# Kernel optimization log

Measured on AMD Instinct MI355X. Metric: run time of the kernel, lower is better.

Reference implementation:

```python
import jax, jax.numpy as jnp
import numpy as np

N, E, C5, C6, H = 50000, 100000, 8000, 12000, 128
RE, R5, R6 = 2 * E, 5 * C5, 6 * C6
BN_EPS = 1e-5


def _bn_relu(x, g, b):
    # BatchNorm1d (training-mode batch stats, biased var) + ReLU
    m = x.mean(0)
    xc = x - m
    v = (xc * xc).mean(0)
    return jax.nn.relu(xc * jax.lax.rsqrt(v + BN_EPS) * g + b)


def _mlp2(x, w1, g1, b1, w2, g2, b2):
    h = _bn_relu(x @ w1, g1, b1)
    return _bn_relu(h @ w2, g2, b2)


def _gather11(x, src_nodes, src_inst, n_inst, tgt_nodes):
    # ptens 1b->1b gather (channel multiplier 2):
    #  part A: identity map on shared atoms, summed over overlapping sources
    #  part B: broadcast of source-instance sum to shared atoms
    pa = jax.ops.segment_sum(x, src_nodes, num_segments=N)[tgt_nodes]
    s = jax.ops.segment_sum(x, src_inst, num_segments=n_inst)
    pb = jax.ops.segment_sum(s[src_inst], src_nodes, num_segments=N)[tgt_nodes]
    return jnp.concatenate([pa, pb], -1)


def _forward(node_rep, edge_rep, cycle_rep, edge_nodes, c5_nodes, c6_nodes, P):
    (nm_w1, nm_g1, nm_b1, nm_w2, nm_g2, nm_b2,
     em_w1, em_g1, em_b1, em_w2, em_g2, em_b2,
     ce_w1, ce_g1, ce_b1, ce_w2, ce_g2, ce_b2,
     cm_w1, cm_g1, cm_b1, cm_w2, cm_g2, cm_b2,
     fm_w, fm_g, fm_b) = P
    edge_inst = jnp.arange(RE, dtype=jnp.int32) // 2
    c5_inst = jnp.arange(R5, dtype=jnp.int32) // 5
    c6_inst = jnp.arange(R6, dtype=jnp.int32) // 6
    cyc_nodes = jnp.concatenate([c5_nodes, c6_nodes])
    cyc_inst = jnp.concatenate([c5_inst, c6_inst + C5])

    # ---- Edge_node ----
    n2e = node_rep[edge_nodes]                                        # 0b->1b(edge), h
    n2e = _gather11(n2e, edge_nodes, edge_inst, E, edge_nodes)        # 2h
    e2e = _gather11(edge_rep, edge_nodes, edge_inst, E, edge_nodes)   # 2h
    e2e = _gather11(e2e, edge_nodes, edge_inst, E, edge_nodes)        # 4h
    e2n = jax.ops.segment_sum(jnp.concatenate([e2e, n2e], -1), edge_nodes, num_segments=N)  # 1b->0b, 6h
    edge_out1 = _mlp2(jnp.concatenate([edge_rep, e2e, n2e], -1),
                      em_w1, em_g1, em_b1, em_w2, em_g2, em_b2)       # [RE, h]
    node_out = _mlp2(jnp.concatenate([node_rep, e2n], -1),
                     nm_w1, nm_g1, nm_b1, nm_w2, nm_g2, nm_b2)        # [N, h]

    # ---- Edge_Cycle ----
    e2c5 = _gather11(edge_rep, edge_nodes, edge_inst, E, c5_nodes)    # 2h
    e2c5 = _gather11(e2c5, c5_nodes, c5_inst, C5, c5_nodes)           # 4h
    e2c6 = _gather11(edge_rep, edge_nodes, edge_inst, E, c6_nodes)    # 2h
    e2c6 = _gather11(e2c6, c6_nodes, c6_inst, C6, c6_nodes)           # 4h
    cycle_in = jnp.concatenate([e2c5, e2c6], 0)                       # row-cat: [R5+R6, 4h]
    cycle_new = jnp.concatenate([cycle_in, cycle_rep], -1)            # 5h
    c2e = _gather11(cycle_new, cyc_nodes, cyc_inst, C5 + C6, edge_nodes)  # 10h
    edge_out2 = _mlp2(jnp.concatenate([edge_rep, c2e], -1),
                      ce_w1, ce_g1, ce_b1, ce_w2, ce_g2, ce_b2)       # [RE, h]
    cycle_out = _mlp2(cycle_new, cm_w1, cm_g1, cm_b1, cm_w2, cm_g2, cm_b2)  # [R5+R6, h]

    edge_out = _bn_relu(jnp.concatenate([edge_out1, edge_out2], -1) @ fm_w, fm_g, fm_b)
    return node_out, edge_out, cycle_out


def setup_inputs() -> dict:
    key = jax.random.key(0)
    ks = jax.random.split(key, 16)
    d = {}
    d["node_rep"] = jax.random.normal(ks[0], (N, H), jnp.float32)
    d["edge_rep"] = jax.random.normal(ks[1], (RE, H), jnp.float32)
    d["cycle_rep"] = jax.random.normal(ks[2], (R5 + R6, H), jnp.float32)
    d["edge_nodes"] = jax.random.randint(ks[3], (RE,), 0, N, jnp.int32)
    d["c5_nodes"] = jax.random.randint(ks[4], (R5,), 0, N, jnp.int32)
    d["c6_nodes"] = jax.random.randint(ks[5], (R6,), 0, N, jnp.int32)
    i = [6]
    def w(shape):
        out = jax.random.normal(ks[i[0]], shape, jnp.float32) / np.float32(np.sqrt(shape[0]))
        i[0] += 1
        return out
    for p, fin in (("nm", 7 * H), ("em", 7 * H), ("ce", 11 * H), ("cm", 5 * H)):
        d[p + "_w1"] = w((fin, 2 * H)); d[p + "_g1"] = jnp.ones((2 * H,), jnp.float32); d[p + "_b1"] = jnp.zeros((2 * H,), jnp.float32)
        d[p + "_w2"] = w((2 * H, H)); d[p + "_g2"] = jnp.ones((H,), jnp.float32); d[p + "_b2"] = jnp.zeros((H,), jnp.float32)
    d["fm_w"] = w((2 * H, H)); d["fm_g"] = jnp.ones((H,), jnp.float32); d["fm_b"] = jnp.zeros((H,), jnp.float32)
    return d


def reference(node_rep, edge_rep, cycle_rep, edge_nodes, c5_nodes, c6_nodes,
              nm_w1, nm_g1, nm_b1, nm_w2, nm_g2, nm_b2,
              em_w1, em_g1, em_b1, em_w2, em_g2, em_b2,
              ce_w1, ce_g1, ce_b1, ce_w2, ce_g2, ce_b2,
              cm_w1, cm_g1, cm_b1, cm_w2, cm_g2, cm_b2,
              fm_w, fm_g, fm_b):
    P = (nm_w1, nm_g1, nm_b1, nm_w2, nm_g2, nm_b2,
         em_w1, em_g1, em_b1, em_w2, em_g2, em_b2,
         ce_w1, ce_g1, ce_b1, ce_w2, ce_g2, ce_b2,
         cm_w1, cm_g1, cm_b1, cm_w2, cm_g2, cm_b2,
         fm_w, fm_g, fm_b)
    return _forward(node_rep, edge_rep, cycle_rep, edge_nodes, c5_nodes, c6_nodes, P)
```

## Files before the change

kernel.cpp:

```cpp
#include <hip/hip_runtime.h>
#include <cstdint>
#include <cstddef>
#include <initializer_list>

typedef short bf16x8 __attribute__((ext_vector_type(8)));
typedef float f32x4 __attribute__((ext_vector_type(4)));

__device__ inline float bf2f(unsigned short h) { return __uint_as_float(((unsigned)h) << 16); }
__device__ inline unsigned short f2bf(float f) {
  unsigned u = __float_as_uint(f);
  u += 0x7fff + ((u >> 16) & 1);
  return (unsigned short)(u >> 16);
}

struct Seg { const void* base; const int* idx; const float* scale; int ld; int wk; int bf16;
             const float* bnsc; const float* bnsh; };
struct GemmArgs { Seg segs[7]; const float* addB; const int* addIdx; float* stats; int addBf16; };

__global__ void k_count(float* dst, const int* __restrict__ idx, int R) {
  int r = blockIdx.x * 256 + threadIdx.x;
  if (r < R) atomicAdd(&dst[idx[r]], 1.0f);
}

__global__ void k_scales(const float* __restrict__ deg, const float* __restrict__ d5,
                         const float* __restrict__ d6, float* deg2, float* dd, int n) {
  int i = blockIdx.x * 256 + threadIdx.x;
  if (i < n) {
    float d = deg[i]; deg2[i] = d * d;
    float a = d5[i], b = d6[i]; dd[i] = a * a + b * b;
  }
}

__global__ void k_wtrans(const float* __restrict__ W, unsigned short* __restrict__ Wt,
                         int K, int CN) {
  int t = blockIdx.x * 256 + threadIdx.x;
  if (t >= K * CN) return;
  int k = t / CN, n = t - k * CN;
  Wt[(size_t)n * K + k] = f2bf(W[t]);
}

__global__ void k_cvt(unsigned short* __restrict__ dst, const float* __restrict__ src, int n8) {
  int i = blockIdx.x * 256 + threadIdx.x;
  if (i >= n8) return;
  const float4* s = (const float4*)(src + (size_t)i * 8);
  float4 a = s[0], b = s[1];
  union { unsigned short u[8]; uint4 v; } o;
  o.u[0] = f2bf(a.x); o.u[1] = f2bf(a.y); o.u[2] = f2bf(a.z); o.u[3] = f2bf(a.w);
  o.u[4] = f2bf(b.x); o.u[5] = f2bf(b.y); o.u[6] = f2bf(b.z); o.u[7] = f2bf(b.w);
  *(uint4*)(dst + (size_t)i * 8) = o.v;
}

__global__ void k_gsum(float* __restrict__ out, int outLd,
                       const float* __restrict__ T, int tLd,
                       const float* __restrict__ scale, const int* __restrict__ idx,
                       int k, int nInst) {
  int t = blockIdx.x * 256 + threadIdx.x;
  int c = t >> 7, ch = t & 127;
  if (c >= nInst) return;
  float acc = 0.f;
  int b0 = c * k;
  for (int j = 0; j < k; ++j) {
    int rid = idx ? idx[b0 + j] : b0 + j;
    float v = T[(size_t)rid * tLd + ch];
    if (scale) v *= scale[rid];
    acc += v;
  }
  out[(size_t)c * outLd + ch] = acc;
}

__global__ void k_gsc(float* __restrict__ dst, const float* __restrict__ T1,
                      const float* __restrict__ T2, const int* __restrict__ gidx,
                      const int* __restrict__ sidx, int k, int nInst, int cshift) {
  int t = blockIdx.x * 256 + threadIdx.x;
  int c = t >> cshift;
  int C = 1 << cshift;
  int ch = t & (C - 1);
  if (c >= nInst) return;
  const float* T = (ch < 128) ? T1 : T2;
  int ch7 = ch & 127;
  float acc = 0.f;
  int b0 = c * k;
  for (int j = 0; j < k; ++j) {
    int rid = gidx ? gidx[b0 + j] : b0 + j;
    acc += T[(size_t)rid * 128 + ch7];
  }
  for (int j = 0; j < k; ++j)
    atomicAdd(&dst[(size_t)sidx[b0 + j] * C + ch], acc);
}

__global__ void k_scatter(float* __restrict__ dst, const float* __restrict__ src,
                          const int* __restrict__ idx, int R, int C, int div) {
  int r = blockIdx.x;
  if (r >= R) return;
  int n = idx[r];
  const float* s = src + (size_t)(r / div) * C;
  float* d = dst + (size_t)n * C;
  for (int c = threadIdx.x; c < C; c += blockDim.x)
    atomicAdd(&d[c], s[c]);
}

__global__ void k_bnfin(float* __restrict__ coef, const float* __restrict__ stats,
                        const float* __restrict__ g, const float* __restrict__ b,
                        int M, int C) {
  int c = threadIdx.x;
  if (c >= C) return;
  float s = 0.f, q = 0.f;
  for (int sh = 0; sh < 16; ++sh) { s += stats[sh * 512 + c]; q += stats[sh * 512 + 256 + c]; }
  float inv = 1.f / (float)M;
  float m = s * inv;
  float v = q * inv - m * m;
  float sc = g[c] * rsqrtf(v + 1e-5f);
  coef[c] = sc;
  coef[C + c] = b[c] - m * sc;
}

template <int OUT_BF16>
__launch_bounds__(256)
__global__ void k_gemm(GemmArgs ga, const unsigned short* __restrict__ Wt, int Ktot,
                       int K, int CN, void* __restrict__ Cp, int M) {
  __shared__ char AsB[2 * 128 * 64];
  __shared__ char BsB[2 * 128 * 64];
  int tid = threadIdx.x;
  int row0 = blockIdx.x * 128, col0 = blockIdx.y * 128;
  int l = tid & 63, w = tid >> 6;
  int wm = w >> 1, wn = w & 1;
  int lr = l & 15, g = l >> 4;
  int chunkOff = (g ^ ((lr >> 1) & 3)) << 4;
  int sm = tid >> 2;
  int sc4 = tid & 3;
  f32x4 acc[4][4] = {};

  uint4 pa0[2], pa1[2], pb[2];
  float psc[2];
  float4 c0, c1, c2, c3;

  auto issue = [&](int k0n) {
    Seg sg = ga.segs[k0n >> 7];
    int kin = k0n & 127;
#pragma unroll
    for (int h = 0; h < 2; ++h) {
      int m = sm + 64 * h;
      int grow = row0 + m;
      uint4 z4 = make_uint4(0, 0, 0, 0);
      pa0[h] = z4; pa1[h] = z4; psc[h] = 1.f;
      if (grow < M) {
        int rid = sg.idx ? sg.idx[grow] : grow;
        if (sg.bf16) {
          pa0[h] = *(const uint4*)((const unsigned short*)sg.base + (size_t)rid * sg.ld + kin + sc4 * 8);
        } else {
          const float* fp = (const float*)sg.base + (size_t)rid * sg.ld + kin + sc4 * 8;
          pa0[h] = *(const uint4*)fp;
          pa1[h] = *(const uint4*)(fp + 4);
          if (sg.scale) psc[h] = sg.scale[rid];
        }
      }
      pb[h] = *(const uint4*)(Wt + (size_t)(col0 + m) * Ktot + sg.wk + kin + sc4 * 8);
    }
    if (sg.bnsc) {
      const float* sp = sg.bnsc + kin + sc4 * 8;
      const float* hp = sg.bnsh + kin + sc4 * 8;
      c0 = *(const float4*)sp; c1 = *(const float4*)(sp + 4);
      c2 = *(const float4*)hp; c3 = *(const float4*)(hp + 4);
    }
  };

  issue(0);
  int buf = 0;
  for (int k0 = 0; k0 < K; k0 += 32) {
    {
      Seg sg = ga.segs[k0 >> 7];
      char* sA = AsB + buf * 8192;
      char* sB = BsB + buf * 8192;
#pragma unroll
      for (int h = 0; h < 2; ++h) {
        int m = sm + 64 * h;
        uint4 pk;
        if (sg.bf16) {
          pk = pa0[h];
          if (sg.bnsc) {
            unsigned short* u = (unsigned short*)&pk;
            float cs0[8] = {c0.x, c0.y, c0.z, c0.w, c1.x, c1.y, c1.z, c1.w};
            float sh0[8] = {c2.x, c2.y, c2.z, c2.w, c3.x, c3.y, c3.z, c3.w};
#pragma unroll
            for (int e = 0; e < 8; ++e) {
              float f = fmaxf(0.f, bf2f(u[e]) * cs0[e] + sh0[e]);
              u[e] = f2bf(f);
            }
          }
        } else {
          float4 v0 = *(const float4*)&pa0[h];
          float4 v1 = *(const float4*)&pa1[h];
          float s = psc[h];
          v0.x *= s; v0.y *= s; v0.z *= s; v0.w *= s;
          v1.x *= s; v1.y *= s; v1.z *= s; v1.w *= s;
          if (sg.bnsc) {
            v0.x = fmaxf(0.f, v0.x * c0.x + c2.x);
            v0.y = fmaxf(0.f, v0.y * c0.y + c2.y);
            v0.z = fmaxf(0.f, v0.z * c0.z + c2.z);
            v0.w = fmaxf(0.f, v0.w * c0.w + c2.w);
            v1.x = fmaxf(0.f, v1.x * c1.x + c3.x);
            v1.y = fmaxf(0.f, v1.y * c1.y + c3.y);
            v1.z = fmaxf(0.f, v1.z * c1.z + c3.z);
            v1.w = fmaxf(0.f, v1.w * c1.w + c3.w);
          }
          pk.x = f2bf(v0.x) | ((unsigned)f2bf(v0.y) << 16);
          pk.y = f2bf(v0.z) | ((unsigned)f2bf(v0.w) << 16);
          pk.z = f2bf(v1.x) | ((unsigned)f2bf(v1.y) << 16);
          pk.w = f2bf(v1.z) | ((unsigned)f2bf(v1.w) << 16);
        }
        *(uint4*)(sA + m * 64 + ((sc4 ^ ((m >> 1) & 3)) << 4)) = pk;
        *(uint4*)(sB + m * 64 + ((sc4 ^ ((m >> 1) & 3)) << 4)) = pb[h];
      }
    }
    __syncthreads();
    if (k0 + 32 < K) issue(k0 + 32);
    const char* lA = AsB + buf * 8192;
    const char* lB = BsB + buf * 8192;
    bf16x8 a[4], b4[4];
#pragma unroll
    for (int i = 0; i < 4; ++i) {
      int m = wm * 64 + i * 16 + lr;
      a[i] = *(const bf16x8*)(lA + m * 64 + chunkOff);
    }
#pragma unroll
    for (int j = 0; j < 4; ++j) {
      int n = wn * 64 + j * 16 + lr;
      b4[j] = *(const bf16x8*)(lB + n * 64 + chunkOff);
    }
#pragma unroll
    for (int i = 0; i < 4; ++i)
#pragma unroll
      for (int j = 0; j < 4; ++j)
        acc[i][j] = __builtin_amdgcn_mfma_f32_16x16x32_bf16(a[i], b4[j], acc[i][j], 0, 0, 0);
    buf ^= 1;
  }

  float csum[4] = {0.f, 0.f, 0.f, 0.f}, cqum[4] = {0.f, 0.f, 0.f, 0.f};
#pragma unroll
  for (int i = 0; i < 4; ++i) {
#pragma unroll
    for (int r = 0; r < 4; ++r) {
      int grow = row0 + wm * 64 + i * 16 + g * 4 + r;
      if (grow >= M) continue;
      const float* zrF = nullptr;
      const unsigned short* zrH = nullptr;
      if (ga.addB) {
        int rid = ga.addIdx ? ga.addIdx[grow] : grow;
        if (ga.addBf16) zrH = (const unsigned short*)ga.addB + (size_t)rid * 256;
        else            zrF = ga.addB + (size_t)rid * 256;
      }
#pragma unroll
      for (int j = 0; j < 4; ++j) {
        int col = col0 + wn * 64 + j * 16 + lr;
        float o = acc[i][j][r];
        if (zrF) o += zrF[col];
        if (zrH) o += bf2f(zrH[col]);
        csum[j] += o; cqum[j] += o * o;
        if (OUT_BF16) ((unsigned short*)Cp)[(size_t)grow * CN + col] = f2bf(o);
        else          ((float*)Cp)[(size_t)grow * CN + col] = o;
      }
    }
  }
  if (ga.stats) {
    int shard = (blockIdx.x & 15) * 512;
#pragma unroll
    for (int j = 0; j < 4; ++j) {
      float s = csum[j], q = cqum[j];
      s += __shfl_xor(s, 16); q += __shfl_xor(q, 16);
      s += __shfl_xor(s, 32); q += __shfl_xor(q, 32);
      if (g == 0) {
        int col = col0 + wn * 64 + j * 16 + lr;
        atomicAdd(&ga.stats[shard + col], s);
        atomicAdd(&ga.stats[shard + 256 + col], q);
      }
    }
  }
}

template <int SB, int DB>
__global__ void k_bnapply(void* __restrict__ dst, const void* __restrict__ yv,
                          const float* __restrict__ coef, int M, int C) {
  int t = blockIdx.x * 256 + threadIdx.x;
  if (t >= M * C) return;
  int c = t & (C - 1);
  float x = SB ? bf2f(((const unsigned short*)yv)[t]) : ((const float*)yv)[t];
  x = x * coef[c] + coef[C + c];
  x = x > 0.f ? x : 0.f;
  if (DB) ((unsigned short*)dst)[t] = f2bf(x);
  else    ((float*)dst)[t] = x;
}

extern "C" void kernel_launch(void* const* d_in, const int* in_sizes, int n_in,
                              void* d_out, int out_size, void* d_ws, size_t ws_size,
                              hipStream_t stream) {
  constexpr int N = 50000, E = 100000, C5 = 8000, C6 = 12000;
  constexpr int RE = 2 * E, R5 = 5 * C5, R6 = 6 * C6, NC = R5 + R6, CC = C5 + C6;

  const float* node_rep  = (const float*)d_in[0];
  const float* edge_rep  = (const float*)d_in[1];
  const float* cycle_rep = (const float*)d_in[2];
  const int* en  = (const int*)d_in[3];
  const int* cn5 = (const int*)d_in[4];
  const int* cn6 = (const int*)d_in[5];
  const float* nm_w1 = (const float*)d_in[6],  *nm_g1 = (const float*)d_in[7],  *nm_b1 = (const float*)d_in[8];
  const float* nm_w2 = (const float*)d_in[9],  *nm_g2 = (const float*)d_in[10], *nm_b2 = (const float*)d_in[11];
  const float* em_w1 = (const float*)d_in[12], *em_g1 = (const float*)d_in[13], *em_b1 = (const float*)d_in[14];
  const float* em_w2 = (const float*)d_in[15], *em_g2 = (const float*)d_in[16], *em_b2 = (const float*)d_in[17];
  const float* ce_w1 = (const float*)d_in[18], *ce_g1 = (const float*)d_in[19], *ce_b1 = (const float*)d_in[20];
  const float* ce_w2 = (const float*)d_in[21], *ce_g2 = (const float*)d_in[22], *ce_b2 = (const float*)d_in[23];
  const float* cm_w1 = (const float*)d_in[24], *cm_g1 = (const float*)d_in[25], *cm_b1 = (const float*)d_in[26];
  const float* cm_w2 = (const float*)d_in[27], *cm_g2 = (const float*)d_in[28], *cm_b2 = (const float*)d_in[29];
  const float* fm_w  = (const float*)d_in[30], *fm_g  = (const float*)d_in[31], *fm_b  = (const float*)d_in[32];
  float* outD = (float*)d_out;
  float* outN = outD;
  float* outE = outD + (size_t)N * 128;
  float* outC = outD + (size_t)(N + RE) * 128;

  char* wsb = (char*)d_ws;
  size_t off = 0;
  auto A = [&](size_t bytes) { void* p = wsb + off; off += (bytes + 255) & ~(size_t)255; return p; };
  float* deg = (float*)A(N * 4);
  float* d5  = (float*)A(N * 4);
  float* d6  = (float*)A(N * 4);
  float* Ae  = (float*)A((size_t)N * 128 * 4);
  float* Be  = (float*)A((size_t)N * 128 * 4);
  float* Bn  = (float*)A((size_t)N * 128 * 4);
  float* pb2 = (float*)A((size_t)N * 256 * 4);
  float* pb5 = (float*)A((size_t)N * 256 * 4);
  float* pb6 = (float*)A((size_t)N * 256 * 4);
  float* Ac  = (float*)A((size_t)N * 128 * 4);
  size_t zeroBytes = off;
  float* deg2 = (float*)A(N * 4);
  float* dd   = (float*)A(N * 4);
  float* Z    = (float*)A((size_t)N * 256 * 4);
  float* stats = (float*)A(16 * 512 * 4);
  float* coefCe1 = (float*)A(512 * 4);
  float* coefCe2 = (float*)A(512 * 4);
  float* coefEm1 = (float*)A(512 * 4);
  float* coefEm2 = (float*)A(512 * 4);
  float* coefNm1 = (float*)A(512 * 4);
  float* coefNm2 = (float*)A(512 * 4);
  float* coefCm1 = (float*)A(512 * 4);
  float* coefCm2 = (float*)A(512 * 4);
  float* coefFm  = (float*)A(512 * 4);
  unsigned short* WtNm1 = (unsigned short*)A((size_t)896 * 256 * 2);
  unsigned short* WtEm1 = (unsigned short*)A((size_t)896 * 256 * 2);
  unsigned short* WtCe1 = (unsigned short*)A((size_t)1408 * 256 * 2);
  unsigned short* WtCm1 = (unsigned short*)A((size_t)640 * 256 * 2);
  unsigned short* WtNm2 = (unsigned short*)A((size_t)256 * 128 * 2);
  unsigned short* WtEm2 = (unsigned short*)A((size_t)256 * 128 * 2);
  unsigned short* WtCe2 = (unsigned short*)A((size_t)256 * 128 * 2);
  unsigned short* WtCm2 = (unsigned short*)A((size_t)256 * 128 * 2);
  unsigned short* WtFm  = (unsigned short*)A((size_t)256 * 128 * 2);
  char*  Yb   = (char*)A((size_t)RE * 256 * 2);
  unsigned short* O2 = (unsigned short*)A((size_t)RE * 128 * 2);
  if (off > ws_size) return;

  unsigned short* Zb = (unsigned short*)Ac;

  float* scb = (float*)Yb;
  float* Ysc = scb + (size_t)CC * 640;

  auto gsum = [&](float* o, int oLd, const float* T, int tLd,
                  const float* scl, const int* idx, int k, int nInst) {
    int tot = nInst * 128;
    k_gsum<<<(tot + 255) / 256, 256, 0, stream>>>(o, oLd, T, tLd, scl, idx, k, nInst);
  };
  auto gsc = [&](float* dst, const float* T1, const float* T2, const int* gidx,
                 const int* sidx, int k, int nInst) {
    int cshift = T2 ? 8 : 7;
    int tot = nInst << cshift;
    k_gsc<<<(tot + 255) / 256, 256, 0, stream>>>(dst, T1, T2, gidx, sidx, k, nInst, cshift);
  };
  auto scat = [&](float* dst, const float* src, const int* idx, int R, int C, int dv) {
    k_scatter<<<R, 128, 0, stream>>>(dst, src, idx, R, C, dv);
  };
  auto wtr = [&](const float* W, unsigned short* Wt, int K, int CN) {
    k_wtrans<<<(K * CN + 255) / 256, 256, 0, stream>>>(W, Wt, K, CN);
  };
  auto gemm = [&](std::initializer_list<Seg> segs, const unsigned short* Wt, int Ktot,
                  int CN, void* Co, int M, bool outBf, const float* addB, const int* addIdx,
                  int addBf, float* st) {
    GemmArgs ga{}; int i = 0;
    for (const Seg& s : segs) ga.segs[i++] = s;
    ga.addB = addB; ga.addIdx = addIdx; ga.stats = st; ga.addBf16 = addBf;
    int K = i * 128;
    dim3 g((M + 127) / 128, CN / 128);
    if (outBf) k_gemm<1><<<g, 256, 0, stream>>>(ga, Wt, Ktot, K, CN, Co, M);
    else       k_gemm<0><<<g, 256, 0, stream>>>(ga, Wt, Ktot, K, CN, Co, M);
  };
  auto zstat = [&]() { hipMemsetAsync(stats, 0, 16 * 512 * sizeof(float), stream); };
  auto fin = [&](float* coef, const float* g, const float* b, int M, int C) {
    k_bnfin<<<1, 256, 0, stream>>>(coef, stats, g, b, M, C);
  };
  auto apply = [&](void* dst, const void* y, const float* coef, int M, int C, int sb, int db) {
    int tot = M * C, gb = (tot + 255) / 256;
    if (sb && db)       k_bnapply<1, 1><<<gb, 256, 0, stream>>>(dst, y, coef, M, C);
    else if (sb && !db) k_bnapply<1, 0><<<gb, 256, 0, stream>>>(dst, y, coef, M, C);
    else if (!sb && db) k_bnapply<0, 1><<<gb, 256, 0, stream>>>(dst, y, coef, M, C);
    else                k_bnapply<0, 0><<<gb, 256, 0, stream>>>(dst, y, coef, M, C);
  };

  hipMemsetAsync(d_ws, 0, zeroBytes, stream);
  k_count<<<(RE + 255) / 256, 256, 0, stream>>>(deg, en, RE);
  k_count<<<(R5 + 255) / 256, 256, 0, stream>>>(d5, cn5, R5);
  k_count<<<(R6 + 255) / 256, 256, 0, stream>>>(d6, cn6, R6);
  k_scales<<<(N + 255) / 256, 256, 0, stream>>>(deg, d5, d6, deg2, dd, N);
  wtr(nm_w1, WtNm1, 896, 256);  wtr(em_w1, WtEm1, 896, 256);
  wtr(ce_w1, WtCe1, 1408, 256); wtr(cm_w1, WtCm1, 640, 256);
  wtr(nm_w2, WtNm2, 256, 128);  wtr(em_w2, WtEm2, 256, 128);
  wtr(ce_w2, WtCe2, 256, 128);  wtr(cm_w2, WtCm2, 256, 128);
  wtr(fm_w,  WtFm,  256, 128);

  scat(Ae, edge_rep, en, RE, 128, 1);
  gsc(Be, edge_rep, nullptr, nullptr, en, 2, E);
  gsc(Bn, node_rep, nullptr, en, en, 2, E);
  gsc(pb2, Ae, Be, en, en, 2, E);

  gsc(pb5, Ae, Be, cn5, cn5, 5, C5);
  gsc(pb6, Ae, Be, cn6, cn6, 6, C6);
  scat(Ac, cycle_rep, cn5, R5, 128, 1);
  scat(Ac, cycle_rep + (size_t)R5 * 128, cn6, R6, 128, 1);

  gsum(scb + 0,   640, Ae, 128, d5, cn5, 5, C5);
  gsum(scb + 128, 640, Be, 128, d5, cn5, 5, C5);
  gsum(scb + 256, 640, pb5, 256, nullptr, cn5, 5, C5);
  gsum(scb + 384, 640, pb5 + 128, 256, nullptr, cn5, 5, C5);
  gsum(scb + 512, 640, cycle_rep, 128, nullptr, nullptr, 5, C5);
  float* sc6 = scb + (size_t)C5 * 640;
  gsum(sc6 + 0,   640, Ae, 128, d6, cn6, 6, C6);
  gsum(sc6 + 128, 640, Be, 128, d6, cn6, 6, C6);
  gsum(sc6 + 256, 640, pb6, 256, nullptr, cn6, 6, C6);
  gsum(sc6 + 384, 640, pb6 + 128, 256, nullptr, cn6, 6, C6);
  gsum(sc6 + 512, 640, cycle_rep + (size_t)R5 * 128, 128, nullptr, nullptr, 6, C6);
  gemm({{scb, nullptr, nullptr, 640, 768, 0}, {scb + 128, nullptr, nullptr, 640, 896, 0},
        {scb + 256, nullptr, nullptr, 640, 1024, 0}, {scb + 384, nullptr, nullptr, 640, 1152, 0},
        {scb + 512, nullptr, nullptr, 640, 1280, 0}},
       WtCe1, 1408, 256, Ysc, CC, false, nullptr, nullptr, 0, nullptr);
  gemm({{Ae, nullptr, dd, 128, 128, 0}, {Be, nullptr, dd, 128, 256, 0},
        {pb5, nullptr, d5, 256, 384, 0}, {pb5 + 128, nullptr, d5, 256, 512, 0},
        {pb6, nullptr, d6, 256, 384, 0}, {pb6 + 128, nullptr, d6, 256, 512, 0},
        {Ac, nullptr, nullptr, 128, 640, 0}},
       WtCe1, 1408, 256, Z, N, false, nullptr, nullptr, 0, nullptr);
  scat(Z, Ysc, cn5, R5, 256, 5);
  scat(Z, Ysc + (size_t)C5 * 256, cn6, R6, 256, 6);
  k_cvt<<<(N * 256 / 8 + 255) / 256, 256, 0, stream>>>(Zb, Z, N * 256 / 8);
  zstat();
  gemm({{edge_rep, nullptr, nullptr, 128, 0, 0}}, WtCe1, 1408, 256, Yb, RE, true,
       (const float*)Zb, en, 1, stats);
  fin(coefCe1, ce_g1, ce_b1, RE, 256);
  zstat();
  gemm({{Yb, nullptr, nullptr, 256, 0, 1, coefCe1, coefCe1 + 256},
        {Yb + 256, nullptr, nullptr, 256, 128, 1, coefCe1 + 128, coefCe1 + 384}},
       WtCe2, 256, 128, O2, RE, true, nullptr, nullptr, 0, stats);
  fin(coefCe2, ce_g2, ce_b2, RE, 128);

  gemm({{Ae, nullptr, deg, 128, 128, 0}, {Be, nullptr, deg, 128, 256, 0},
        {pb2, nullptr, nullptr, 256, 384, 0}, {pb2 + 128, nullptr, nullptr, 256, 512, 0},
        {node_rep, nullptr, deg, 128, 640, 0}, {Bn, nullptr, nullptr, 128, 768, 0}},
       WtEm1, 896, 256, Zb, N, true, nullptr, nullptr, 0, nullptr);
  zstat();
  gemm({{edge_rep, nullptr, nullptr, 128, 0, 0}}, WtEm1, 896, 256, Yb, RE, true,
       (const float*)Zb, en, 1, stats);
  fin(coefEm1, em_g1, em_b1, RE, 256);
  zstat();
  gemm({{Yb, nullptr, nullptr, 256, 0, 1, coefEm1, coefEm1 + 256},
        {Yb + 256, nullptr, nullptr, 256, 128, 1, coefEm1 + 128, coefEm1 + 384}},
       WtEm2, 256, 128, outE, RE, false, nullptr, nullptr, 0, stats);
  fin(coefEm2, em_g2, em_b2, RE, 128);

  zstat();
  gemm({{node_rep, nullptr, nullptr, 128, 0, 0}, {Ae, nullptr, deg2, 128, 128, 0},
        {Be, nullptr, deg2, 128, 256, 0}, {pb2, nullptr, deg, 256, 384, 0},
        {pb2 + 128, nullptr, deg, 256, 512, 0}, {node_rep, nullptr, deg2, 128, 640, 0},
        {Bn, nullptr, deg, 128, 768, 0}},
       WtNm1, 896, 256, Yb, N, true, nullptr, nullptr, 0, stats);
  fin(coefNm1, nm_g1, nm_b1, N, 256);
  zstat();
  gemm({{Yb, nullptr, nullptr, 256, 0, 1, coefNm1, coefNm1 + 256},
        {Yb + 256, nullptr, nullptr, 256, 128, 1, coefNm1 + 128, coefNm1 + 384}},
       WtNm2, 256, 128, outN, N, false, nullptr, nullptr, 0, stats);
  fin(coefNm2, nm_g2, nm_b2, N, 128);
  apply(outN, outN, coefNm2, N, 128, 0, 0);

  gemm({{Ae, nullptr, d5, 128, 0, 0}, {Be, nullptr, d5, 128, 128, 0},
        {pb5, nullptr, nullptr, 256, 256, 0}, {pb5 + 128, nullptr, nullptr, 256, 384, 0}},
       WtCm1, 640, 256, Zb, N, true, nullptr, nullptr, 0, nullptr);
  zstat();
  gemm({{cycle_rep, nullptr, nullptr, 128, 512, 0}}, WtCm1, 640, 256, Yb, R5, true,
       (const float*)Zb, cn5, 1, stats);
  gemm({{Ae, nullptr, d6, 128, 0, 0}, {Be, nullptr, d6, 128, 128, 0},
        {pb6, nullptr, nullptr, 256, 256, 0}, {pb6 + 128, nullptr, nullptr, 256, 384, 0}},
       WtCm1, 640, 256, Zb, N, true, nullptr, nullptr, 0, nullptr);
  gemm({{cycle_rep + (size_t)R5 * 128, nullptr, nullptr, 128, 512, 0}}, WtCm1, 640, 256,
       Yb + (size_t)R5 * 256 * 2, R6, true, (const float*)Zb, cn6, 1, stats);
  fin(coefCm1, cm_g1, cm_b1, NC, 256);
  zstat();
  gemm({{Yb, nullptr, nullptr, 256, 0, 1, coefCm1, coefCm1 + 256},
        {Yb + 256, nullptr, nullptr, 256, 128, 1, coefCm1 + 128, coefCm1 + 384}},
       WtCm2, 256, 128, outC, NC, false, nullptr, nullptr, 0, stats);
  fin(coefCm2, cm_g2, cm_b2, NC, 128);
  apply(outC, outC, coefCm2, NC, 128, 0, 0);

  zstat();
  gemm({{outE, nullptr, nullptr, 128, 0, 0, coefEm2, coefEm2 + 128},
        {O2, nullptr, nullptr, 128, 128, 1, coefCe2, coefCe2 + 128}},
       WtFm, 256, 128, Yb, RE, true, nullptr, nullptr, 0, stats);
  fin(coefFm, fm_g, fm_b, RE, 128);
  apply(outE, Yb, coefFm, RE, 128, 1, 0);
}
```

Baseline: 2.871 ms.

## Build CSR adjacency and replace atomic scatters with gather kernels in bf16

After: 2.796 ms. 2.6% less time.

```diff
diff --git a/kernel.cpp b/kernel.cpp
--- a/kernel.cpp
+++ b/kernel.cpp
@@ -17,17 +17,48 @@
              const float* bnsc; const float* bnsh; };
 struct GemmArgs { Seg segs[7]; const float* addB; const int* addIdx; float* stats; int addBf16; };
 
-__global__ void k_count(float* dst, const int* __restrict__ idx, int R) {
+__global__ void k_hist(int* cnt, const int* __restrict__ idx, int R) {
   int r = blockIdx.x * 256 + threadIdx.x;
-  if (r < R) atomicAdd(&dst[idx[r]], 1.0f);
-}
-
-__global__ void k_scales(const float* __restrict__ deg, const float* __restrict__ d5,
-                         const float* __restrict__ d6, float* deg2, float* dd, int n) {
+  if (r < R) atomicAdd(&cnt[idx[r]], 1);
+}
+
+__global__ void k_scan(int* __restrict__ cnt, int* __restrict__ off, int n) {
+  __shared__ int part[1024];
+  int t = threadIdx.x;
+  int chunk = (n + 1023) >> 10;
+  int b0 = t * chunk, b1 = min(n, b0 + chunk);
+  int s = 0;
+  for (int i = b0; i < b1; ++i) s += cnt[i];
+  part[t] = s;
+  __syncthreads();
+  for (int d = 1; d < 1024; d <<= 1) {
+    int v = (t >= d) ? part[t - d] : 0;
+    __syncthreads();
+    part[t] += v;
+    __syncthreads();
+  }
+  int run = t ? part[t - 1] : 0;
+  for (int i = b0; i < b1; ++i) { off[i] = run; run += cnt[i]; cnt[i] = 0; }
+  if (t == 1023) off[n] = part[1023];
+}
+
+__global__ void k_fill(int* __restrict__ adj, int* __restrict__ cur,
+                       const int* __restrict__ off, const int* __restrict__ idx, int R) {
+  int r = blockIdx.x * 256 + threadIdx.x;
+  if (r >= R) return;
+  int n = idx[r];
+  int p = atomicAdd(&cur[n], 1);
+  adj[off[n] + p] = r;
+}
+
+__global__ void k_scales(const int* __restrict__ ce, const int* __restrict__ c5,
+                         const int* __restrict__ c6, float* deg, float* d5, float* d6,
+                         float* deg2, float* dd, int n) {
   int i = blockIdx.x * 256 + threadIdx.x;
   if (i < n) {
-    float d = deg[i]; deg2[i] = d * d;
-    float a = d5[i], b = d6[i]; dd[i] = a * a + b * b;
+    float d = (float)ce[i]; deg[i] = d; deg2[i] = d * d;
+    float a = (float)c5[i], b = (float)c6[i];
+    d5[i] = a; d6[i] = b; dd[i] = a * a + b * b;
   }
 }
 
@@ -50,8 +81,9 @@
   *(uint4*)(dst + (size_t)i * 8) = o.v;
 }
 
-__global__ void k_gsum(float* __restrict__ out, int outLd,
-                       const float* __restrict__ T, int tLd,
+template <int SBF>
+__global__ void k_gsum(unsigned short* __restrict__ out, int outLd,
+                       const void* __restrict__ T, int tLd,
                        const float* __restrict__ scale, const int* __restrict__ idx,
                        int k, int nInst) {
   int t = blockIdx.x * 256 + threadIdx.x;
@@ -61,42 +93,114 @@
   int b0 = c * k;
   for (int j = 0; j < k; ++j) {
     int rid = idx ? idx[b0 + j] : b0 + j;
-    float v = T[(size_t)rid * tLd + ch];
+    float v = SBF ? bf2f(((const unsigned short*)T)[(size_t)rid * tLd + ch])
+                  : ((const float*)T)[(size_t)rid * tLd + ch];
     if (scale) v *= scale[rid];
     acc += v;
   }
-  out[(size_t)c * outLd + ch] = acc;
-}
-
-__global__ void k_gsc(float* __restrict__ dst, const float* __restrict__ T1,
-                      const float* __restrict__ T2, const int* __restrict__ gidx,
-                      const int* __restrict__ sidx, int k, int nInst, int cshift) {
-  int t = blockIdx.x * 256 + threadIdx.x;
-  int c = t >> cshift;
-  int C = 1 << cshift;
-  int ch = t & (C - 1);
-  if (c >= nInst) return;
-  const float* T = (ch < 128) ? T1 : T2;
+  out[(size_t)c * outLd + ch] = f2bf(acc);
+}
+
+__global__ void k_csr_ae(unsigned short* __restrict__ out, const float* __restrict__ src,
+                         const int* __restrict__ off, const int* __restrict__ adj, int n) {
+  int t = blockIdx.x * 256 + threadIdx.x;
+  int node = t >> 7, ch = t & 127;
+  if (node >= n) return;
+  float a = 0.f;
+  int p0 = off[node], p1 = off[node + 1];
+  for (int p = p0; p < p1; ++p) a += src[(size_t)adj[p] * 128 + ch];
+  out[(size_t)node * 128 + ch] = f2bf(a);
+}
+
+__global__ void k_csr_be(unsigned short* __restrict__ out, const float* __restrict__ src,
+                         const int* __restrict__ off, const int* __restrict__ adj, int n) {
+  int t = blockIdx.x * 256 + threadIdx.x;
+  int node = t >> 7, ch = t & 127;
+  if (node >= n) return;
+  float a = 0.f;
+  int p0 = off[node], p1 = off[node + 1];
+  for (int p = p0; p < p1; ++p) {
+    int e2 = adj[p] & ~1;
+    a += src[(size_t)e2 * 128 + ch] + src[(size_t)(e2 + 1) * 128 + ch];
+  }
+  out[(size_t)node * 128 + ch] = f2bf(a);
+}
+
+__global__ void k_csr_bn(unsigned short* __restrict__ out, const float* __restrict__ src,
+                         const int* __restrict__ en, const int* __restrict__ off,
+                         const int* __restrict__ adj, int n) {
+  int t = blockIdx.x * 256 + threadIdx.x;
+  int node = t >> 7, ch = t & 127;
+  if (node >= n) return;
+  float a = 0.f;
+  int p0 = off[node], p1 = off[node + 1];
+  for (int p = p0; p < p1; ++p) {
+    int e2 = adj[p] & ~1;
+    a += src[(size_t)en[e2] * 128 + ch] + src[(size_t)en[e2 + 1] * 128 + ch];
+  }
+  out[(size_t)node * 128 + ch] = f2bf(a);
+}
+
+__global__ void k_csr_p2(unsigned short* __restrict__ out, const unsigned short* __restrict__ AeB,
+                         const unsigned short* __restrict__ BeB, const int* __restrict__ en,
+                         const int* __restrict__ off, const int* __restrict__ adj, int n) {
+  int t = blockIdx.x * 256 + threadIdx.x;
+  int node = t >> 8, ch = t & 255;
+  if (node >= n) return;
+  const unsigned short* Tab = (ch < 128) ? AeB : BeB;
   int ch7 = ch & 127;
-  float acc = 0.f;
-  int b0 = c * k;
-  for (int j = 0; j < k; ++j) {
-    int rid = gidx ? gidx[b0 + j] : b0 + j;
-    acc += T[(size_t)rid * 128 + ch7];
-  }
-  for (int j = 0; j < k; ++j)
-    atomicAdd(&dst[(size_t)sidx[b0 + j] * C + ch], acc);
-}
-
-__global__ void k_scatter(float* __restrict__ dst, const float* __restrict__ src,
-                          const int* __restrict__ idx, int R, int C, int div) {
-  int r = blockIdx.x;
-  if (r >= R) return;
-  int n = idx[r];
-  const float* s = src + (size_t)(r / div) * C;
-  float* d = dst + (size_t)n * C;
-  for (int c = threadIdx.x; c < C; c += blockDim.x)
-    atomicAdd(&d[c], s[c]);
+  float a = 0.f;
+  int p0 = off[node], p1 = off[node + 1];
+  for (int p = p0; p < p1; ++p) {
+    int e2 = adj[p] & ~1;
+    a += bf2f(Tab[(size_t)en[e2] * 128 + ch7]) + bf2f(Tab[(size_t)en[e2 + 1] * 128 + ch7]);
+  }
+  out[(size_t)node * 256 + ch] = f2bf(a);
+}
+
+template <int KK>
+__global__ void k_csr_p56(unsigned short* __restrict__ out, const unsigned short* __restrict__ AeB,
+                          const unsigned short* __restrict__ BeB, const int* __restrict__ cn,
+                          const int* __restrict__ off, const int* __restrict__ adj, int n) {
+  int t = blockIdx.x * 256 + threadIdx.x;
+  int node = t >> 8, ch = t & 255;
+  if (node >= n) return;
+  const unsigned short* Tab = (ch < 128) ? AeB : BeB;
+  int ch7 = ch & 127;
+  float a = 0.f;
+  int p0 = off[node], p1 = off[node + 1];
+  for (int p = p0; p < p1; ++p) {
+    int b = (adj[p] / KK) * KK;
+#pragma unroll
+    for (int j = 0; j < KK; ++j) a += bf2f(Tab[(size_t)cn[b + j] * 128 + ch7]);
+  }
+  out[(size_t)node * 256 + ch] = f2bf(a);
+}
+
+__global__ void k_csr_ac(unsigned short* __restrict__ out, const float* __restrict__ cyc,
+                         const int* __restrict__ off5, const int* __restrict__ adj5,
+                         const int* __restrict__ off6, const int* __restrict__ adj6,
+                         int r5off, int n) {
+  int t = blockIdx.x * 256 + threadIdx.x;
+  int node = t >> 7, ch = t & 127;
+  if (node >= n) return;
+  float a = 0.f;
+  for (int p = off5[node]; p < off5[node + 1]; ++p) a += cyc[(size_t)adj5[p] * 128 + ch];
+  for (int p = off6[node]; p < off6[node + 1]; ++p) a += cyc[(size_t)(r5off + adj6[p]) * 128 + ch];
+  out[(size_t)node * 128 + ch] = f2bf(a);
+}
+
+__global__ void k_zmerge(unsigned short* __restrict__ Zb, const float* __restrict__ Ysc5,
+                         const float* __restrict__ Ysc6,
+                         const int* __restrict__ off5, const int* __restrict__ adj5,
+                         const int* __restrict__ off6, const int* __restrict__ adj6, int n) {
+  int t = blockIdx.x * 256 + threadIdx.x;
+  int node = t >> 8, ch = t & 255;
+  if (node >= n) return;
+  float a = bf2f(Zb[(size_t)node * 256 + ch]);
+  for (int p = off5[node]; p < off5[node + 1]; ++p) a += Ysc5[(size_t)(adj5[p] / 5) * 256 + ch];
+  for (int p = off6[node]; p < off6[node + 1]; ++p) a += Ysc6[(size_t)(adj6[p] / 6) * 256 + ch];
+  Zb[(size_t)node * 256 + ch] = f2bf(a);
 }
 
 __global__ void k_bnfin(float* __restrict__ coef, const float* __restrict__ stats,
@@ -147,6 +251,7 @@
         int rid = sg.idx ? sg.idx[grow] : grow;
         if (sg.bf16) {
           pa0[h] = *(const uint4*)((const unsigned short*)sg.base + (size_t)rid * sg.ld + kin + sc4 * 8);
+          if (sg.scale) psc[h] = sg.scale[rid];
         } else {
           const float* fp = (const float*)sg.base + (size_t)rid * sg.ld + kin + sc4 * 8;
           pa0[h] = *(const uint4*)fp;
@@ -186,6 +291,11 @@
               float f = fmaxf(0.f, bf2f(u[e]) * cs0[e] + sh0[e]);
               u[e] = f2bf(f);
             }
+          } else if (sg.scale) {
+            unsigned short* u = (unsigned short*)&pk;
+            float s = psc[h];
+#pragma unroll
+            for (int e = 0; e < 8; ++e) u[e] = f2bf(bf2f(u[e]) * s);
           }
         } else {
           float4 v0 = *(const float4*)&pa0[h];
@@ -319,20 +429,21 @@
   char* wsb = (char*)d_ws;
   size_t off = 0;
   auto A = [&](size_t bytes) { void* p = wsb + off; off += (bytes + 255) & ~(size_t)255; return p; };
-  float* deg = (float*)A(N * 4);
-  float* d5  = (float*)A(N * 4);
-  float* d6  = (float*)A(N * 4);
-  float* Ae  = (float*)A((size_t)N * 128 * 4);
-  float* Be  = (float*)A((size_t)N * 128 * 4);
-  float* Bn  = (float*)A((size_t)N * 128 * 4);
-  float* pb2 = (float*)A((size_t)N * 256 * 4);
-  float* pb5 = (float*)A((size_t)N * 256 * 4);
-  float* pb6 = (float*)A((size_t)N * 256 * 4);
-  float* Ac  = (float*)A((size_t)N * 128 * 4);
-  size_t zeroBytes = off;
+  float* deg  = (float*)A(N * 4);
+  float* d5   = (float*)A(N * 4);
+  float* d6   = (float*)A(N * 4);
   float* deg2 = (float*)A(N * 4);
   float* dd   = (float*)A(N * 4);
-  float* Z    = (float*)A((size_t)N * 256 * 4);
+  int* cntE = (int*)A(N * 4);
+  int* cnt5 = (int*)A(N * 4);
+  int* cnt6 = (int*)A(N * 4);
+  size_t cntBytes = (char*)A(0) - (char*)cntE;
+  int* offE = (int*)A((N + 1) * 4);
+  int* off5 = (int*)A((N + 1) * 4);
+  int* off6 = (int*)A((N + 1) * 4);
+  int* adjE = (int*)A((size_t)RE * 4);
+  int* adj5 = (int*)A((size_t)R5 * 4);
+  int* adj6 = (int*)A((size_t)R6 * 4);
   float* stats = (float*)A(16 * 512 * 4);
   float* coefCe1 = (float*)A(512 * 4);
   float* coefCe2 = (float*)A(512 * 4);
@@ -352,31 +463,36 @@
   unsigned short* WtCe2 = (unsigned short*)A((size_t)256 * 128 * 2);
   unsigned short* WtCm2 = (unsigned short*)A((size_t)256 * 128 * 2);
   unsigned short* WtFm  = (unsigned short*)A((size_t)256 * 128 * 2);
+  unsigned short* AeB  = (unsigned short*)A((size_t)N * 128 * 2);
+  unsigned short* BeB  = (unsigned short*)A((size_t)N * 128 * 2);
+  unsigned short* BnB  = (unsigned short*)A((size_t)N * 128 * 2);
+  unsigned short* AcB  = (unsigned short*)A((size_t)N * 128 * 2);
+  unsigned short* pb2B = (unsigned short*)A((size_t)N * 256 * 2);
+  unsigned short* pb5B = (unsigned short*)A((size_t)N * 256 * 2);
+  unsigned short* pb6B = (unsigned short*)A((size_t)N * 256 * 2);
+  unsigned short* Zb   = (unsigned short*)A((size_t)N * 256 * 2);
+  unsigned short* edgeB = (unsigned short*)A((size_t)RE * 128 * 2);
+  unsigned short* nodeB = (unsigned short*)A((size_t)N * 128 * 2);
+  unsigned short* cycB  = (unsigned short*)A((size_t)NC * 128 * 2);
+  unsigned short* Eb    = (unsigned short*)A((size_t)RE * 128 * 2);
   char*  Yb   = (char*)A((size_t)RE * 256 * 2);
   unsigned short* O2 = (unsigned short*)A((size_t)RE * 128 * 2);
   if (off > ws_size) return;
 
-  unsigned short* Zb = (unsigned short*)Ac;
-
-  float* scb = (float*)Yb;
-  float* Ysc = scb + (size_t)CC * 640;
-
-  auto gsum = [&](float* o, int oLd, const float* T, int tLd,
-                  const float* scl, const int* idx, int k, int nInst) {
+  unsigned short* scbB = (unsigned short*)Yb;
+  float* Ysc = (float*)(Yb + (size_t)CC * 640 * 2);
+
+  auto gsumB = [&](unsigned short* o, int oLd, const unsigned short* T, int tLd,
+                   const float* scl, const int* idx, int k, int nInst) {
     int tot = nInst * 128;
-    k_gsum<<<(tot + 255) / 256, 256, 0, stream>>>(o, oLd, T, tLd, scl, idx, k, nInst);
-  };
-  auto gsc = [&](float* dst, const float* T1, const float* T2, const int* gidx,
-                 const int* sidx, int k, int nInst) {
-    int cshift = T2 ? 8 : 7;
-    int tot = nInst << cshift;
-    k_gsc<<<(tot + 255) / 256, 256, 0, stream>>>(dst, T1, T2, gidx, sidx, k, nInst, cshift);
-  };
-  auto scat = [&](float* dst, const float* src, const int* idx, int R, int C, int dv) {
-    k_scatter<<<R, 128, 0, stream>>>(dst, src, idx, R, C, dv);
+    k_gsum<1><<<(tot + 255) / 256, 256, 0, stream>>>(o, oLd, T, tLd, scl, idx, k, nInst);
   };
   auto wtr = [&](const float* W, unsigned short* Wt, int K, int CN) {
     k_wtrans<<<(K * CN + 255) / 256, 256, 0, stream>>>(W, Wt, K, CN);
+  };
+  auto cvt = [&](unsigned short* dst, const float* src, size_t elems) {
+    int n8 = (int)(elems / 8);
+    k_cvt<<<(n8 + 255) / 256, 256, 0, stream>>>(dst, src, n8);
   };
   auto gemm = [&](std::initializer_list<Seg> segs, const unsigned short* Wt, int Ktot,
                   int CN, void* Co, int M, bool outBf, const float* addB, const int* addIdx,
@@ -401,52 +517,61 @@
     else                k_bnapply<0, 0><<<gb, 256, 0, stream>>>(dst, y, coef, M, C);
   };
 
-  hipMemsetAsync(d_ws, 0, zeroBytes, stream);
-  k_count<<<(RE + 255) / 256, 256, 0, stream>>>(deg, en, RE);
-  k_count<<<(R5 + 255) / 256, 256, 0, stream>>>(d5, cn5, R5);
-  k_count<<<(R6 + 255) / 256, 256, 0, stream>>>(d6, cn6, R6);
-  k_scales<<<(N + 255) / 256, 256, 0, stream>>>(deg, d5, d6, deg2, dd, N);
+  hipMemsetAsync(cntE, 0, cntBytes, stream);
+  k_hist<<<(RE + 255) / 256, 256, 0, stream>>>(cntE, en, RE);
+  k_hist<<<(R5 + 255) / 256, 256, 0, stream>>>(cnt5, cn5, R5);
+  k_hist<<<(R6 + 255) / 256, 256, 0, stream>>>(cnt6, cn6, R6);
+  k_scales<<<(N + 255) / 256, 256, 0, stream>>>(cntE, cnt5, cnt6, deg, d5, d6, deg2, dd, N);
+  k_scan<<<1, 1024, 0, stream>>>(cntE, offE, N);
+  k_scan<<<1, 1024, 0, stream>>>(cnt5, off5, N);
+  k_scan<<<1, 1024, 0, stream>>>(cnt6, off6, N);
+  k_fill<<<(RE + 255) / 256, 256, 0, stream>>>(adjE, cntE, offE, en, RE);
+  k_fill<<<(R5 + 255) / 256, 256, 0, stream>>>(adj5, cnt5, off5, cn5, R5);
+  k_fill<<<(R6 + 255) / 256, 256, 0, stream>>>(adj6, cnt6, off6, cn6, R6);
   wtr(nm_w1, WtNm1, 896, 256);  wtr(em_w1, WtEm1, 896, 256);
   wtr(ce_w1, WtCe1, 1408, 256); wtr(cm_w1, WtCm1, 640, 256);
   wtr(nm_w2, WtNm2, 256, 128);  wtr(em_w2, WtEm2, 256, 128);
   wtr(ce_w2, WtCe2, 256, 128);  wtr(cm_w2, WtCm2, 256, 128);
   wtr(fm_w,  WtFm,  256, 128);
-
-  scat(Ae, edge_rep, en, RE, 128, 1);
-  gsc(Be, edge_rep, nullptr, nullptr, en, 2, E);
-  gsc(Bn, node_rep, nullptr, en, en, 2, E);
-  gsc(pb2, Ae, Be, en, en, 2, E);
-
-  gsc(pb5, Ae, Be, cn5, cn5, 5, C5);
-  gsc(pb6, Ae, Be, cn6, cn6, 6, C6);
-  scat(Ac, cycle_rep, cn5, R5, 128, 1);
-  scat(Ac, cycle_rep + (size_t)R5 * 128, cn6, R6, 128, 1);
-
-  gsum(scb + 0,   640, Ae, 128, d5, cn5, 5, C5);
-  gsum(scb + 128, 640, Be, 128, d5, cn5, 5, C5);
-  gsum(scb + 256, 640, pb5, 256, nullptr, cn5, 5, C5);
-  gsum(scb + 384, 640, pb5 + 128, 256, nullptr, cn5, 5, C5);
-  gsum(scb + 512, 640, cycle_rep, 128, nullptr, nullptr, 5, C5);
-  float* sc6 = scb + (size_t)C5 * 640;
-  gsum(sc6 + 0,   640, Ae, 128, d6, cn6, 6, C6);
-  gsum(sc6 + 128, 640, Be, 128, d6, cn6, 6, C6);
-  gsum(sc6 + 256, 640, pb6, 256, nullptr, cn6, 6, C6);
-  gsum(sc6 + 384, 640, pb6 + 128, 256, nullptr, cn6, 6, C6);
-  gsum(sc6 + 512, 640, cycle_rep + (size_t)R5 * 128, 128, nullptr, nullptr, 6, C6);
-  gemm({{scb, nullptr, nullptr, 640, 768, 0}, {scb + 128, nullptr, nullptr, 640, 896, 0},
-        {scb + 256, nullptr, nullptr, 640, 1024, 0}, {scb + 384, nullptr, nullptr, 640, 1152, 0},
-        {scb + 512, nullptr, nullptr, 640, 1280, 0}},
+  cvt(edgeB, edge_rep, (size_t)RE * 128);
+  cvt(nodeB, node_rep, (size_t)N * 128);
+  cvt(cycB,  cycle_rep, (size_t)NC * 128);
+
+  {
+    int g128 = (N * 128 + 255) / 256, g256 = (N * 256 + 255) / 256;
+    k_csr_ae<<<g128, 256, 0, stream>>>(AeB, edge_rep, offE, adjE, N);
+    k_csr_be<<<g128, 256, 0, stream>>>(BeB, edge_rep, offE, adjE, N);
+    k_csr_bn<<<g128, 256, 0, stream>>>(BnB, node_rep, en, offE, adjE, N);
+    k_csr_ac<<<g128, 256, 0, stream>>>(AcB, cycle_rep, off5, adj5, off6, adj6, R5, N);
+    k_csr_p2<<<g256, 256, 0, stream>>>(pb2B, AeB, BeB, en, offE, adjE, N);
+    k_csr_p56<5><<<g256, 256, 0, stream>>>(pb5B, AeB, BeB, cn5, off5, adj5, N);
+    k_csr_p56<6><<<g256, 256, 0, stream>>>(pb6B, AeB, BeB, cn6, off6, adj6, N);
+  }
+
+  gsumB(scbB + 0,   640, AeB, 128, d5, cn5, 5, C5);
+  gsumB(scbB + 128, 640, BeB, 128, d5, cn5, 5, C5);
+  gsumB(scbB + 256, 640, pb5B, 256, nullptr, cn5, 5, C5);
+  gsumB(scbB + 384, 640, pb5B + 128, 256, nullptr, cn5, 5, C5);
+  gsumB(scbB + 512, 640, cycB, 128, nullptr, nullptr, 5, C5);
+  unsigned short* sc6B = scbB + (size_t)C5 * 640;
+  gsumB(sc6B + 0,   640, AeB, 128, d6, cn6, 6, C6);
+  gsumB(sc6B + 128, 640, BeB, 128, d6, cn6, 6, C6);
+  gsumB(sc6B + 256, 640, pb6B, 256, nullptr, cn6, 6, C6);
+  gsumB(sc6B + 384, 640, pb6B + 128, 256, nullptr, cn6, 6, C6);
+  gsumB(sc6B + 512, 640, cycB + (size_t)R5 * 128, 128, nullptr, nullptr, 6, C6);
+  gemm({{scbB, nullptr, nullptr, 640, 768, 1}, {scbB + 128, nullptr, nullptr, 640, 896, 1},
+        {scbB + 256, nullptr, nullptr, 640, 1024, 1}, {scbB + 384, nullptr, nullptr, 640, 1152, 1},
+        {scbB + 512, nullptr, nullptr, 640, 1280, 1}},
        WtCe1, 1408, 256, Ysc, CC, false, nullptr, nullptr, 0, nullptr);
-  gemm({{Ae, nullptr, dd, 128, 128, 0}, {Be, nullptr, dd, 128, 256, 0},
-        {pb5, nullptr, d5, 256, 384, 0}, {pb5 + 128, nullptr, d5, 256, 512, 0},
-        {pb6, nullptr, d6, 256, 384, 0}, {pb6 + 128, nullptr, d6, 256, 512, 0},
-        {Ac, nullptr, nullptr, 128, 640, 0}},
-       WtCe1, 1408, 256, Z, N, false, nullptr, nullptr, 0, nullptr);
-  scat(Z, Ysc, cn5, R5, 256, 5);
-  scat(Z, Ysc + (size_t)C5 * 256, cn6, R6, 256, 6);
-  k_cvt<<<(N * 256 / 8 + 255) / 256, 256, 0, stream>>>(Zb, Z, N * 256 / 8);
-  zstat();
-  gemm({{edge_rep, nullptr, nullptr, 128, 0, 0}}, WtCe1, 1408, 256, Yb, RE, true,
+  gemm({{AeB, nullptr, dd, 128, 128, 1}, {BeB, nullptr, dd, 128, 256, 1},
+        {pb5B, nullptr, d5, 256, 384, 1}, {pb5B + 128, nullptr, d5, 256, 512, 1},
+        {pb6B, nullptr, d6, 256, 384, 1}, {pb6B + 128, nullptr, d6, 256, 512, 1},
+        {AcB, nullptr, nullptr, 128, 640, 1}},
+       WtCe1, 1408, 256, Zb, N, true, nullptr, nullptr, 0, nullptr);
+  k_zmerge<<<(N * 256 + 255) / 256, 256, 0, stream>>>(
+      Zb, Ysc, Ysc + (size_t)C5 * 256, off5, adj5, off6, adj6, N);
+  zstat();
+  gemm({{edgeB, nullptr, nullptr, 128, 0, 1}}, WtCe1, 1408, 256, Yb, RE, true,
        (const float*)Zb, en, 1, stats);
   fin(coefCe1, ce_g1, ce_b1, RE, 256);
   zstat();
@@ -455,25 +580,25 @@
        WtCe2, 256, 128, O2, RE, true, nullptr, nullptr, 0, stats);
   fin(coefCe2, ce_g2, ce_b2, RE, 128);
 
-  gemm({{Ae, nullptr, deg, 128, 128, 0}, {Be, nullptr, deg, 128, 256, 0},
-        {pb2, nullptr, nullptr, 256, 384, 0}, {pb2 + 128, nullptr, nullptr, 256, 512, 0},
-        {node_rep, nullptr, deg, 128, 640, 0}, {Bn, nullptr, nullptr, 128, 768, 0}},
+  gemm({{AeB, nullptr, deg, 128, 128, 1}, {BeB, nullptr, deg, 128, 256, 1},
+        {pb2B, nullptr, nullptr, 256, 384, 1}, {pb2B + 128, nullptr, nullptr, 256, 512, 1},
+        {nodeB, nullptr, deg, 128, 640, 1}, {BnB, nullptr, nullptr, 128, 768, 1}},
        WtEm1, 896, 256, Zb, N, true, nullptr, nullptr, 0, nullptr);
   zstat();
-  gemm({{edge_rep, nullptr, nullptr, 128, 0, 0}}, WtEm1, 896, 256, Yb, RE, true,
+  gemm({{edgeB, nullptr, nullptr, 128, 0, 1}}, WtEm1, 896, 256, Yb, RE, true,
        (const float*)Zb, en, 1, stats);
   fin(coefEm1, em_g1, em_b1, RE, 256);
   zstat();
   gemm({{Yb, nullptr, nullptr, 256, 0, 1, coefEm1, coefEm1 + 256},
         {Yb + 256, nullptr, nullptr, 256, 128, 1, coefEm1 + 128, coefEm1 + 384}},
-       WtEm2, 256, 128, outE, RE, false, nullptr, nullptr, 0, stats);
+       WtEm2, 256, 128, Eb, RE, true, nullptr, nullptr, 0, stats);
   fin(coefEm2, em_g2, em_b2, RE, 128);
 
   zstat();
-  gemm({{node_rep, nullptr, nullptr, 128, 0, 0}, {Ae, nullptr, deg2, 128, 128, 0},
-        {Be, nullptr, deg2, 128, 256, 0}, {pb2, nullptr, deg, 256, 384, 0},
-        {pb2 + 128, nullptr, deg, 256, 512, 0}, {node_rep, nullptr, deg2, 128, 640, 0},
-        {Bn, nullptr, deg, 128, 768, 0}},
+  gemm({{nodeB, nullptr, nullptr, 128, 0, 1}, {AeB, nullptr, deg2, 128, 128, 1},
+        {BeB, nullptr, deg2, 128, 256, 1}, {pb2B, nullptr, deg, 256, 384, 1},
+        {pb2B + 128, nullptr, deg, 256, 512, 1}, {nodeB, nullptr, deg2, 128, 640, 1},
+        {BnB, nullptr, deg, 128, 768, 1}},
        WtNm1, 896, 256, Yb, N, true, nullptr, nullptr, 0, stats);
   fin(coefNm1, nm_g1, nm_b1, N, 256);
   zstat();
@@ -483,16 +608,16 @@
   fin(coefNm2, nm_g2, nm_b2, N, 128);
   apply(outN, outN, coefNm2, N, 128, 0, 0);
 
-  gemm({{Ae, nullptr, d5, 128, 0, 0}, {Be, nullptr, d5, 128, 128, 0},
-        {pb5, nullptr, nullptr, 256, 256, 0}, {pb5 + 128, nullptr, nullptr, 256, 384, 0}},
+  gemm({{AeB, nullptr, d5, 128, 0, 1}, {BeB, nullptr, d5, 128, 128, 1},
+        {pb5B, nullptr, nullptr, 256, 256, 1}, {pb5B + 128, nullptr, nullptr, 256, 384, 1}},
        WtCm1, 640, 256, Zb, N, true, nullptr, nullptr, 0, nullptr);
   zstat();
-  gemm({{cycle_rep, nullptr, nullptr, 128, 512, 0}}, WtCm1, 640, 256, Yb, R5, true,
+  gemm({{cycB, nullptr, nullptr, 128, 512, 1}}, WtCm1, 640, 256, Yb, R5, true,
        (const float*)Zb, cn5, 1, stats);
-  gemm({{Ae, nullptr, d6, 128, 0, 0}, {Be, nullptr, d6, 128, 128, 0},
-        {pb6, nullptr, nullptr, 256, 256, 0}, {pb6 + 128, nullptr, nullptr, 256, 384, 0}},
+  gemm({{AeB, nullptr, d6, 128, 0, 1}, {BeB, nullptr, d6, 128, 128, 1},
+        {pb6B, nullptr, nullptr, 256, 256, 1}, {pb6B + 128, nullptr, nullptr, 256, 384, 1}},
        WtCm1, 640, 256, Zb, N, true, nullptr, nullptr, 0, nullptr);
-  gemm({{cycle_rep + (size_t)R5 * 128, nullptr, nullptr, 128, 512, 0}}, WtCm1, 640, 256,
+  gemm({{cycB + (size_t)R5 * 128, nullptr, nullptr, 128, 512, 1}}, WtCm1, 640, 256,
        Yb + (size_t)R5 * 256 * 2, R6, true, (const float*)Zb, cn6, 1, stats);
   fin(coefCm1, cm_g1, cm_b1, NC, 256);
   zstat();
@@ -503,7 +628,7 @@
   apply(outC, outC, coefCm2, NC, 128, 0, 0);
 
   zstat();
-  gemm({{outE, nullptr, nullptr, 128, 0, 0, coefEm2, coefEm2 + 128},
+  gemm({{Eb, nullptr, nullptr, 128, 0, 1, coefEm2, coefEm2 + 128},
         {O2, nullptr, nullptr, 128, 128, 1, coefCe2, coefCe2 + 128}},
        WtFm, 256, 128, Yb, RE, true, nullptr, nullptr, 0, stats);
   fin(coefFm, fm_g, fm_b, RE, 128);
```
